# Performance work log

Measured on AMD Instinct MI355X. Metric: run time of the kernel, lower is better.

The kernel has to match this reference:

```python
import jax, jax.numpy as jnp
import numpy as np

B, N, H, E = 4, 256, 128, 32

def setup_inputs() -> dict:
    key = jax.random.key(0)
    ks = jax.random.split(key, 7)
    s = 0.05
    return {
        "node_h": jax.random.normal(ks[0], (B, N, H), dtype=jnp.float32),
        "dart_h": jax.random.normal(ks[1], (B, N, N, H), dtype=jnp.float32),
        "edge_x": jax.random.normal(ks[2], (B, N, N, E), dtype=jnp.float32),
        "W1": jax.random.normal(ks[3], (3 * H + E, H), dtype=jnp.float32) * s,
        "b1": jnp.zeros((H,), dtype=jnp.float32),
        "W2": jax.random.normal(ks[4], (H, H), dtype=jnp.float32) * s,
        "b2": jnp.zeros((H,), dtype=jnp.float32),
    }

def reference(node_h, dart_h, edge_x, W1, b1, W2, b2):
    # Split first-layer weight by concat blocks [src | dst | dart_h | edge_x]
    W1s, W1d, W1h, W1e = W1[:H], W1[H:2*H], W1[2*H:3*H], W1[3*H:]
    # Equivalent to mlp(cat([src_expand, dst_expand, dart_h, edge_x])) but
    # computes the small [B,N,H] matmuls before broadcasting to [B,N,N,H].
    pre = (jnp.einsum('bih,hk->bik', node_h, W1s)[:, :, None, :]
           + jnp.einsum('bjh,hk->bjk', node_h, W1d)[:, None, :, :]
           + jnp.einsum('bijh,hk->bijk', dart_h, W1h)
           + jnp.einsum('bije,ek->bijk', edge_x, W1e)
           + b1)
    h = jax.nn.relu(pre)
    return jnp.einsum('bijh,hk->bijk', h, W2) + b2
```

## Files before the change

kernel.cpp:

```cpp
#include <hip/hip_runtime.h>
#include <hip/hip_bf16.h>


typedef __attribute__((ext_vector_type(8))) short bf16x8;
typedef __attribute__((ext_vector_type(4))) short bf16x4;
typedef __attribute__((ext_vector_type(4))) float f32x4;

__device__ __forceinline__ unsigned short f2bf(float f) {
  union { float f; unsigned u; } v; v.f = f;
  unsigned r = v.u + 0x7FFFu + ((v.u >> 16) & 1u);
  return (unsigned short)(r >> 16);
}

__global__ void prep_kernel(const float* __restrict__ node, const float* __restrict__ W1,
                            const float* __restrict__ b1, const float* __restrict__ W2,
                            float* __restrict__ S, float* __restrict__ DT,
                            unsigned short* __restrict__ W1hT, unsigned short* __restrict__ W1eT,
                            unsigned short* __restrict__ W2T) {
  const int t = threadIdx.x;
  if (blockIdx.x < 256) {
    __shared__ float nrow[4 * 128];
    const int bi0 = blockIdx.x * 4;
    if (t < 128)
      reinterpret_cast<float4*>(nrow)[t] = reinterpret_cast<const float4*>(node + bi0 * 128)[t];
    __syncthreads();
    const int kc = t & 127, half = t >> 7;
    float s0 = 0.f, s1 = 0.f, d0 = 0.f, d1 = 0.f;
    for (int h = 0; h < 128; ++h) {
      float ws = W1[h * 128 + kc];
      float wd = W1[(128 + h) * 128 + kc];
      float n0 = nrow[(half * 2) * 128 + h];
      float n1 = nrow[(half * 2 + 1) * 128 + h];
      s0 = fmaf(n0, ws, s0); s1 = fmaf(n1, ws, s1);
      d0 = fmaf(n0, wd, d0); d1 = fmaf(n1, wd, d1);
    }
    const float bv = b1[kc];
    const int b = bi0 >> 8, i0 = bi0 & 255;
    S[(bi0 + half * 2) * 128 + kc] = s0 + bv;
    S[(bi0 + half * 2 + 1) * 128 + kc] = s1 + bv;
    DT[(b * 128 + kc) * 256 + i0 + half * 2] = d0;
    DT[(b * 128 + kc) * 256 + i0 + half * 2 + 1] = d1;
  } else {
    int gid = (blockIdx.x - 256) * 256 + t;
    for (int idx = gid; idx < 16384; idx += 2048)
      W1hT[idx] = f2bf(W1[(256 + (idx & 127)) * 128 + (idx >> 7)]);
    for (int idx = gid; idx < 4096; idx += 2048)
      W1eT[idx] = f2bf(W1[(384 + (idx & 31)) * 128 + (idx >> 5)]);
    for (int idx = gid; idx < 16384; idx += 2048)
      W2T[idx] = f2bf(W2[(idx & 127) * 128 + (idx >> 7)]);
  }
}

#define LDD 136
#define LDE 40

__launch_bounds__(256, 2)
__global__ void fused_kernel(const float* __restrict__ dart, const float* __restrict__ edge,
                             const float* __restrict__ S, const float* __restrict__ DT,
                             const unsigned short* __restrict__ W1hT,
                             const unsigned short* __restrict__ W1eT,
                             const unsigned short* __restrict__ W2T,
                             const float* __restrict__ b2, float* __restrict__ out) {
  __shared__ unsigned short sDart[64 * LDD];
  __shared__ unsigned short sEdge[64 * LDE];
  __shared__ unsigned short sH[64 * LDD];

  const int tid = threadIdx.x;
  const int lane = tid & 63;
  const int w = tid >> 6;
  const int g = lane >> 4;
  const int lj = lane & 15;

  const int bi = blockIdx.x;
  const int b = bi >> 8;
  const size_t m_base = (size_t)bi * 256;

  bf16x8 wh[2][4], w2f[4][2], we[2];
#pragma unroll
  for (int kt = 0; kt < 2; ++kt)
#pragma unroll
    for (int hs = 0; hs < 4; ++hs)
      wh[kt][hs] = *reinterpret_cast<const bf16x8*>(&W1hT[(w * 32 + kt * 16 + lj) * 128 + hs * 32 + g * 8]);
#pragma unroll
  for (int kt = 0; kt < 2; ++kt)
    we[kt] = *reinterpret_cast<const bf16x8*>(&W1eT[(w * 32 + kt * 16 + lj) * 32 + g * 8]);
#pragma unroll
  for (int ks = 0; ks < 4; ++ks)
#pragma unroll
    for (int nt = 0; nt < 2; ++nt)
      w2f[ks][nt] = *reinterpret_cast<const bf16x8*>(&W2T[(w * 32 + nt * 16 + lj) * 128 + ks * 32 + g * 8]);

  float sv[2][4], b2v[2][4];
#pragma unroll
  for (int kt = 0; kt < 2; ++kt)
#pragma unroll
    for (int r = 0; r < 4; ++r)
      sv[kt][r] = S[bi * 128 + w * 32 + kt * 16 + g * 4 + r];
#pragma unroll
  for (int nt = 0; nt < 2; ++nt)
#pragma unroll
    for (int r = 0; r < 4; ++r)
      b2v[nt][r] = b2[w * 32 + nt * 16 + g * 4 + r];

  const int srow = tid >> 2;
  const int c0 = (tid & 3) * 32;
  const int e0 = (tid & 3) * 8;

  float4 rD[8], rE[2];

  {
    const float4* dsrc = reinterpret_cast<const float4*>(dart + (m_base + srow) * 128 + c0);
#pragma unroll
    for (int p = 0; p < 8; ++p) rD[p] = dsrc[p];
    const float4* esrc = reinterpret_cast<const float4*>(edge + (m_base + srow) * 32 + e0);
    rE[0] = esrc[0]; rE[1] = esrc[1];
  }
  {
#pragma unroll
    for (int p = 0; p < 4; ++p) {
      float4 a = rD[2 * p], c = rD[2 * p + 1];
      bf16x8 pk;
      pk[0] = (short)f2bf(a.x); pk[1] = (short)f2bf(a.y);
      pk[2] = (short)f2bf(a.z); pk[3] = (short)f2bf(a.w);
      pk[4] = (short)f2bf(c.x); pk[5] = (short)f2bf(c.y);
      pk[6] = (short)f2bf(c.z); pk[7] = (short)f2bf(c.w);
      *reinterpret_cast<bf16x8*>(&sDart[srow * LDD + c0 + p * 8]) = pk;
    }
    float4 a = rE[0], c = rE[1];
    bf16x8 pk;
    pk[0] = (short)f2bf(a.x); pk[1] = (short)f2bf(a.y);
    pk[2] = (short)f2bf(a.z); pk[3] = (short)f2bf(a.w);
    pk[4] = (short)f2bf(c.x); pk[5] = (short)f2bf(c.y);
    pk[6] = (short)f2bf(c.z); pk[7] = (short)f2bf(c.w);
    *reinterpret_cast<bf16x8*>(&sEdge[srow * LDE + e0]) = pk;
  }
  __syncthreads();

  for (int t = 0; t < 4; ++t) {
    const int j0 = t * 64;

    float dv[2][4][4];
    {
      const float* DTp = DT + (size_t)(b * 128 + w * 32) * 256 + j0;
#pragma unroll
      for (int kt = 0; kt < 2; ++kt)
#pragma unroll
        for (int jt = 0; jt < 4; ++jt)
#pragma unroll
          for (int r = 0; r < 4; ++r)
            dv[kt][jt][r] = DTp[(kt * 16 + g * 4 + r) * 256 + jt * 16 + lj];
    }

    if (t < 3) {
      const float4* dsrc = reinterpret_cast<const float4*>(dart + (m_base + j0 + 64 + srow) * 128 + c0);
#pragma unroll
      for (int p = 0; p < 8; ++p) rD[p] = dsrc[p];
      const float4* esrc = reinterpret_cast<const float4*>(edge + (m_base + j0 + 64 + srow) * 32 + e0);
      rE[0] = esrc[0]; rE[1] = esrc[1];
    }

    f32x4 acc1[2][4];
#pragma unroll
    for (int kt = 0; kt < 2; ++kt)
#pragma unroll
      for (int jt = 0; jt < 4; ++jt) acc1[kt][jt] = (f32x4){0.f, 0.f, 0.f, 0.f};

#pragma unroll
    for (int hs = 0; hs < 4; ++hs) {
#pragma unroll
      for (int jt = 0; jt < 4; ++jt) {
        bf16x8 bd = *reinterpret_cast<const bf16x8*>(&sDart[(jt * 16 + lj) * LDD + hs * 32 + g * 8]);
        acc1[0][jt] = __builtin_amdgcn_mfma_f32_16x16x32_bf16(wh[0][hs], bd, acc1[0][jt], 0, 0, 0);
        acc1[1][jt] = __builtin_amdgcn_mfma_f32_16x16x32_bf16(wh[1][hs], bd, acc1[1][jt], 0, 0, 0);
      }
    }
#pragma unroll
    for (int jt = 0; jt < 4; ++jt) {
      bf16x8 be = *reinterpret_cast<const bf16x8*>(&sEdge[(jt * 16 + lj) * LDE + e0 - (tid & 3) * 8 + g * 8]);
      acc1[0][jt] = __builtin_amdgcn_mfma_f32_16x16x32_bf16(we[0], be, acc1[0][jt], 0, 0, 0);
      acc1[1][jt] = __builtin_amdgcn_mfma_f32_16x16x32_bf16(we[1], be, acc1[1][jt], 0, 0, 0);
    }

#pragma unroll
    for (int kt = 0; kt < 2; ++kt) {
#pragma unroll
      for (int jt = 0; jt < 4; ++jt) {
        bf16x4 hp;
#pragma unroll
        for (int r = 0; r < 4; ++r) {
          float x = acc1[kt][jt][r] + sv[kt][r] + dv[kt][jt][r];
          x = x > 0.f ? x : 0.f;
          hp[r] = (short)f2bf(x);
        }
        *reinterpret_cast<bf16x4*>(&sH[(jt * 16 + lj) * LDD + w * 32 + kt * 16 + g * 4]) = hp;
      }
    }
    __syncthreads();

    f32x4 acc2[4][2];
#pragma unroll
    for (int jt = 0; jt < 4; ++jt)
#pragma unroll
      for (int nt = 0; nt < 2; ++nt) acc2[jt][nt] = (f32x4){0.f, 0.f, 0.f, 0.f};

#pragma unroll
    for (int ks = 0; ks < 4; ++ks) {
#pragma unroll
      for (int jt = 0; jt < 4; ++jt) {
        bf16x8 ah = *reinterpret_cast<const bf16x8*>(&sH[(jt * 16 + lj) * LDD + ks * 32 + g * 8]);
        acc2[jt][0] = __builtin_amdgcn_mfma_f32_16x16x32_bf16(w2f[ks][0], ah, acc2[jt][0], 0, 0, 0);
        acc2[jt][1] = __builtin_amdgcn_mfma_f32_16x16x32_bf16(w2f[ks][1], ah, acc2[jt][1], 0, 0, 0);
      }
    }

    if (t < 3) {
#pragma unroll
      for (int p = 0; p < 4; ++p) {
        float4 a = rD[2 * p], c = rD[2 * p + 1];
        bf16x8 pk;
        pk[0] = (short)f2bf(a.x); pk[1] = (short)f2bf(a.y);
        pk[2] = (short)f2bf(a.z); pk[3] = (short)f2bf(a.w);
        pk[4] = (short)f2bf(c.x); pk[5] = (short)f2bf(c.y);
        pk[6] = (short)f2bf(c.z); pk[7] = (short)f2bf(c.w);
        *reinterpret_cast<bf16x8*>(&sDart[srow * LDD + c0 + p * 8]) = pk;
      }
      float4 a = rE[0], c = rE[1];
      bf16x8 pk;
      pk[0] = (short)f2bf(a.x); pk[1] = (short)f2bf(a.y);
      pk[2] = (short)f2bf(a.z); pk[3] = (short)f2bf(a.w);
      pk[4] = (short)f2bf(c.x); pk[5] = (short)f2bf(c.y);
      pk[6] = (short)f2bf(c.z); pk[7] = (short)f2bf(c.w);
      *reinterpret_cast<bf16x8*>(&sEdge[srow * LDE + e0]) = pk;
    }

    {
      float* op = out + (m_base + j0) * 128;
#pragma unroll
      for (int jt = 0; jt < 4; ++jt)
#pragma unroll
        for (int nt = 0; nt < 2; ++nt) {
          float4 v;
          v.x = acc2[jt][nt][0] + b2v[nt][0];
          v.y = acc2[jt][nt][1] + b2v[nt][1];
          v.z = acc2[jt][nt][2] + b2v[nt][2];
          v.w = acc2[jt][nt][3] + b2v[nt][3];
          *reinterpret_cast<float4*>(&op[(size_t)(jt * 16 + lj) * 128 + w * 32 + nt * 16 + g * 4]) = v;
        }
    }
    __syncthreads();
  }
}

extern "C" void kernel_launch(void* const* d_in, const int* in_sizes, int n_in,
                              void* d_out, int out_size, void* d_ws, size_t ws_size,
                              hipStream_t stream) {
  const float* node = (const float*)d_in[0];
  const float* dart = (const float*)d_in[1];
  const float* edge = (const float*)d_in[2];
  const float* W1   = (const float*)d_in[3];
  const float* b1   = (const float*)d_in[4];
  const float* W2   = (const float*)d_in[5];
  const float* b2   = (const float*)d_in[6];
  float* out = (float*)d_out;

  float* S  = (float*)d_ws;
  float* DT = S + 131072;
  unsigned short* W1hT = (unsigned short*)(DT + 131072);
  unsigned short* W1eT = W1hT + 16384;
  unsigned short* W2T  = W1eT + 4096;

  hipLaunchKernelGGL(prep_kernel, dim3(264), dim3(256), 0, stream,
                     node, W1, b1, W2, S, DT, W1hT, W1eT, W2T);
  hipLaunchKernelGGL(fused_kernel, dim3(1024), dim3(256), 0, stream,
                     dart, edge, S, DT, W1hT, W1eT, W2T, b2, out);
}
```

Before: 93.81 us.

## Load dart/edge directly from global into MFMA operands, double-buffer hidden tile

```diff
diff --git a/kernel.cpp b/kernel.cpp
--- a/kernel.cpp
+++ b/kernel.cpp
@@ -10,6 +10,15 @@
   union { float f; unsigned u; } v; v.f = f;
   unsigned r = v.u + 0x7FFFu + ((v.u >> 16) & 1u);
   return (unsigned short)(r >> 16);
+}
+
+__device__ __forceinline__ bf16x8 cvt8(float4 a, float4 b) {
+  bf16x8 r;
+  r[0] = (short)f2bf(a.x); r[1] = (short)f2bf(a.y);
+  r[2] = (short)f2bf(a.z); r[3] = (short)f2bf(a.w);
+  r[4] = (short)f2bf(b.x); r[5] = (short)f2bf(b.y);
+  r[6] = (short)f2bf(b.z); r[7] = (short)f2bf(b.w);
+  return r;
 }
 
 __global__ void prep_kernel(const float* __restrict__ node, const float* __restrict__ W1,
@@ -51,19 +60,16 @@
   }
 }
 
-#define LDD 136
-#define LDE 40
-
-__launch_bounds__(256, 2)
+#define LDH 136
+
+__launch_bounds__(256, 3)
 __global__ void fused_kernel(const float* __restrict__ dart, const float* __restrict__ edge,
                              const float* __restrict__ S, const float* __restrict__ DT,
                              const unsigned short* __restrict__ W1hT,
                              const unsigned short* __restrict__ W1eT,
                              const unsigned short* __restrict__ W2T,
                              const float* __restrict__ b2, float* __restrict__ out) {
-  __shared__ unsigned short sDart[64 * LDD];
-  __shared__ unsigned short sEdge[64 * LDE];
-  __shared__ unsigned short sH[64 * LDD];
+  __shared__ unsigned short sH[2][64 * LDH];
 
   const int tid = threadIdx.x;
   const int lane = tid & 63;
@@ -75,7 +81,7 @@
   const int b = bi >> 8;
   const size_t m_base = (size_t)bi * 256;
 
-  bf16x8 wh[2][4], w2f[4][2], we[2];
+  bf16x8 wh[2][4], we[2];
 #pragma unroll
   for (int kt = 0; kt < 2; ++kt)
 #pragma unroll
@@ -84,11 +90,6 @@
 #pragma unroll
   for (int kt = 0; kt < 2; ++kt)
     we[kt] = *reinterpret_cast<const bf16x8*>(&W1eT[(w * 32 + kt * 16 + lj) * 32 + g * 8]);
-#pragma unroll
-  for (int ks = 0; ks < 4; ++ks)
-#pragma unroll
-    for (int nt = 0; nt < 2; ++nt)
-      w2f[ks][nt] = *reinterpret_cast<const bf16x8*>(&W2T[(w * 32 + nt * 16 + lj) * 128 + ks * 32 + g * 8]);
 
   float sv[2][4], b2v[2][4];
 #pragma unroll
@@ -102,42 +103,33 @@
     for (int r = 0; r < 4; ++r)
       b2v[nt][r] = b2[w * 32 + nt * 16 + g * 4 + r];
 
-  const int srow = tid >> 2;
-  const int c0 = (tid & 3) * 32;
-  const int e0 = (tid & 3) * 8;
-
-  float4 rD[8], rE[2];
-
-  {
-    const float4* dsrc = reinterpret_cast<const float4*>(dart + (m_base + srow) * 128 + c0);
-#pragma unroll
-    for (int p = 0; p < 8; ++p) rD[p] = dsrc[p];
-    const float4* esrc = reinterpret_cast<const float4*>(edge + (m_base + srow) * 32 + e0);
-    rE[0] = esrc[0]; rE[1] = esrc[1];
-  }
-  {
-#pragma unroll
-    for (int p = 0; p < 4; ++p) {
-      float4 a = rD[2 * p], c = rD[2 * p + 1];
-      bf16x8 pk;
-      pk[0] = (short)f2bf(a.x); pk[1] = (short)f2bf(a.y);
-      pk[2] = (short)f2bf(a.z); pk[3] = (short)f2bf(a.w);
-      pk[4] = (short)f2bf(c.x); pk[5] = (short)f2bf(c.y);
-      pk[6] = (short)f2bf(c.z); pk[7] = (short)f2bf(c.w);
-      *reinterpret_cast<bf16x8*>(&sDart[srow * LDD + c0 + p * 8]) = pk;
-    }
-    float4 a = rE[0], c = rE[1];
-    bf16x8 pk;
-    pk[0] = (short)f2bf(a.x); pk[1] = (short)f2bf(a.y);
-    pk[2] = (short)f2bf(a.z); pk[3] = (short)f2bf(a.w);
-    pk[4] = (short)f2bf(c.x); pk[5] = (short)f2bf(c.y);
-    pk[6] = (short)f2bf(c.z); pk[7] = (short)f2bf(c.w);
-    *reinterpret_cast<bf16x8*>(&sEdge[srow * LDE + e0]) = pk;
-  }
-  __syncthreads();
-
   for (int t = 0; t < 4; ++t) {
     const int j0 = t * 64;
+    const float* dbase = dart + (m_base + j0 + lj) * 128 + g * 8;
+    const float* ebase = edge + (m_base + j0 + lj) * 32 + g * 8;
+
+    f32x4 acc1[2][4];
+#pragma unroll
+    for (int kt = 0; kt < 2; ++kt)
+#pragma unroll
+      for (int jt = 0; jt < 4; ++jt) acc1[kt][jt] = (f32x4){0.f, 0.f, 0.f, 0.f};
+
+    float4 c0, c1, n0, n1;
+    c0 = reinterpret_cast<const float4*>(dbase)[0];
+    c1 = reinterpret_cast<const float4*>(dbase)[1];
+#pragma unroll
+    for (int s = 0; s < 16; ++s) {
+      {
+        const float* p = (s < 15) ? (dbase + ((s + 1) & 3) * 2048 + ((s + 1) >> 2) * 32)
+                                  : ebase;
+        n0 = reinterpret_cast<const float4*>(p)[0];
+        n1 = reinterpret_cast<const float4*>(p)[1];
+      }
+      bf16x8 bd = cvt8(c0, c1);
+      acc1[0][s & 3] = __builtin_amdgcn_mfma_f32_16x16x32_bf16(wh[0][s >> 2], bd, acc1[0][s & 3], 0, 0, 0);
+      acc1[1][s & 3] = __builtin_amdgcn_mfma_f32_16x16x32_bf16(wh[1][s >> 2], bd, acc1[1][s & 3], 0, 0, 0);
+      c0 = n0; c1 = n1;
+    }
 
     float dv[2][4][4];
     {
@@ -151,36 +143,20 @@
             dv[kt][jt][r] = DTp[(kt * 16 + g * 4 + r) * 256 + jt * 16 + lj];
     }
 
-    if (t < 3) {
-      const float4* dsrc = reinterpret_cast<const float4*>(dart + (m_base + j0 + 64 + srow) * 128 + c0);
-#pragma unroll
-      for (int p = 0; p < 8; ++p) rD[p] = dsrc[p];
-      const float4* esrc = reinterpret_cast<const float4*>(edge + (m_base + j0 + 64 + srow) * 32 + e0);
-      rE[0] = esrc[0]; rE[1] = esrc[1];
-    }
-
-    f32x4 acc1[2][4];
-#pragma unroll
-    for (int kt = 0; kt < 2; ++kt)
-#pragma unroll
-      for (int jt = 0; jt < 4; ++jt) acc1[kt][jt] = (f32x4){0.f, 0.f, 0.f, 0.f};
-
-#pragma unroll
-    for (int hs = 0; hs < 4; ++hs) {
-#pragma unroll
-      for (int jt = 0; jt < 4; ++jt) {
-        bf16x8 bd = *reinterpret_cast<const bf16x8*>(&sDart[(jt * 16 + lj) * LDD + hs * 32 + g * 8]);
-        acc1[0][jt] = __builtin_amdgcn_mfma_f32_16x16x32_bf16(wh[0][hs], bd, acc1[0][jt], 0, 0, 0);
-        acc1[1][jt] = __builtin_amdgcn_mfma_f32_16x16x32_bf16(wh[1][hs], bd, acc1[1][jt], 0, 0, 0);
-      }
-    }
-#pragma unroll
-    for (int jt = 0; jt < 4; ++jt) {
-      bf16x8 be = *reinterpret_cast<const bf16x8*>(&sEdge[(jt * 16 + lj) * LDE + e0 - (tid & 3) * 8 + g * 8]);
-      acc1[0][jt] = __builtin_amdgcn_mfma_f32_16x16x32_bf16(we[0], be, acc1[0][jt], 0, 0, 0);
-      acc1[1][jt] = __builtin_amdgcn_mfma_f32_16x16x32_bf16(we[1], be, acc1[1][jt], 0, 0, 0);
-    }
-
+#pragma unroll
+    for (int s = 0; s < 4; ++s) {
+      if (s < 3) {
+        const float* p = ebase + (s + 1) * 512;
+        n0 = reinterpret_cast<const float4*>(p)[0];
+        n1 = reinterpret_cast<const float4*>(p)[1];
+      }
+      bf16x8 bd = cvt8(c0, c1);
+      acc1[0][s] = __builtin_amdgcn_mfma_f32_16x16x32_bf16(we[0], bd, acc1[0][s], 0, 0, 0);
+      acc1[1][s] = __builtin_amdgcn_mfma_f32_16x16x32_bf16(we[1], bd, acc1[1][s], 0, 0, 0);
+      c0 = n0; c1 = n1;
+    }
+
+    unsigned short* sHc = sH[t & 1];
 #pragma unroll
     for (int kt = 0; kt < 2; ++kt) {
 #pragma unroll
@@ -192,11 +168,19 @@
           x = x > 0.f ? x : 0.f;
           hp[r] = (short)f2bf(x);
         }
-        *reinterpret_cast<bf16x4*>(&sH[(jt * 16 + lj) * LDD + w * 32 + kt * 16 + g * 4]) = hp;
-      }
-    }
+        *reinterpret_cast<bf16x4*>(&sHc[(jt * 16 + lj) * LDH + w * 32 + kt * 16 + g * 4]) = hp;
+      }
+    }
+
     __syncthreads();
 
+    bf16x8 w2f[4][2];
+#pragma unroll
+    for (int ks = 0; ks < 4; ++ks)
+#pragma unroll
+      for (int nt = 0; nt < 2; ++nt)
+        w2f[ks][nt] = *reinterpret_cast<const bf16x8*>(&W2T[(w * 32 + nt * 16 + lj) * 128 + ks * 32 + g * 8]);
+
     f32x4 acc2[4][2];
 #pragma unroll
     for (int jt = 0; jt < 4; ++jt)
@@ -207,34 +191,14 @@
     for (int ks = 0; ks < 4; ++ks) {
 #pragma unroll
       for (int jt = 0; jt < 4; ++jt) {
-        bf16x8 ah = *reinterpret_cast<const bf16x8*>(&sH[(jt * 16 + lj) * LDD + ks * 32 + g * 8]);
+        bf16x8 ah = *reinterpret_cast<const bf16x8*>(&sHc[(jt * 16 + lj) * LDH + ks * 32 + g * 8]);
         acc2[jt][0] = __builtin_amdgcn_mfma_f32_16x16x32_bf16(w2f[ks][0], ah, acc2[jt][0], 0, 0, 0);
         acc2[jt][1] = __builtin_amdgcn_mfma_f32_16x16x32_bf16(w2f[ks][1], ah, acc2[jt][1], 0, 0, 0);
       }
     }
 
-    if (t < 3) {
-#pragma unroll
-      for (int p = 0; p < 4; ++p) {
-        float4 a = rD[2 * p], c = rD[2 * p + 1];
-        bf16x8 pk;
-        pk[0] = (short)f2bf(a.x); pk[1] = (short)f2bf(a.y);
-        pk[2] = (short)f2bf(a.z); pk[3] = (short)f2bf(a.w);
-        pk[4] = (short)f2bf(c.x); pk[5] = (short)f2bf(c.y);
-        pk[6] = (short)f2bf(c.z); pk[7] = (short)f2bf(c.w);
-        *reinterpret_cast<bf16x8*>(&sDart[srow * LDD + c0 + p * 8]) = pk;
-      }
-      float4 a = rE[0], c = rE[1];
-      bf16x8 pk;
-      pk[0] = (short)f2bf(a.x); pk[1] = (short)f2bf(a.y);
-      pk[2] = (short)f2bf(a.z); pk[3] = (short)f2bf(a.w);
-      pk[4] = (short)f2bf(c.x); pk[5] = (short)f2bf(c.y);
-      pk[6] = (short)f2bf(c.z); pk[7] = (short)f2bf(c.w);
-      *reinterpret_cast<bf16x8*>(&sEdge[srow * LDE + e0]) = pk;
-    }
-
     {
-      float* op = out + (m_base + j0) * 128;
+      float* op = out + (m_base + j0) * 128 + w * 32;
 #pragma unroll
       for (int jt = 0; jt < 4; ++jt)
 #pragma unroll
@@ -244,10 +208,9 @@
           v.y = acc2[jt][nt][1] + b2v[nt][1];
           v.z = acc2[jt][nt][2] + b2v[nt][2];
           v.w = acc2[jt][nt][3] + b2v[nt][3];
-          *reinterpret_cast<float4*>(&op[(size_t)(jt * 16 + lj) * 128 + w * 32 + nt * 16 + g * 4]) = v;
+          *reinterpret_cast<float4*>(&op[(size_t)(jt * 16 + lj) * 128 + nt * 16 + g * 4]) = v;
         }
     }
-    __syncthreads();
   }
 }
 
```

Measured after the change: 231.0 us. 2.46x slower.
